# Kernel tuning notes

Hardware: AMD Instinct MI355X
Metric: run time of the kernel (lower is better)

## Reference

```python
import jax, jax.numpy as jnp
import numpy as np

N, K, GS = 11008, 4096, 128   # outfeatures, infeatures, group_size
INTER, KSTRIDE = 4, 64        # interleave, kstride from pack_intweight
B, S = 4, 2048
NG = K // GS                  # number of quantization groups


def _pack_np(q):
    """Replicates torch pack_intweight on an (N, K) int array of 4-bit values."""
    P = q.reshape(N, K // 32, 32)
    P = P.reshape(N, K // 32, 4, 4, 2).transpose(0, 1, 3, 2, 4).reshape(N, K // 32, 32)
    P = P.reshape(N, K // 32, 4, 8).reshape(N, K // 32, 4, 4, 2)
    P = P.transpose(0, 1, 2, 4, 3).reshape(N, K)
    P = P.reshape(N // INTER, INTER, K // KSTRIDE, KSTRIDE).transpose(0, 2, 1, 3)
    P = P.reshape(N // INTER, K // KSTRIDE, KSTRIDE, INTER)
    P = P[..., 0] | (P[..., 1] << 4) | (P[..., 2] << 8) | (P[..., 3] << 12)
    # uint16 bit pattern stored in int32 (schema has no int16)
    return P.reshape(N // INTER, K).astype(np.int32)


def setup_inputs() -> dict:
    rng = np.random.default_rng(0)
    q_unpacked = rng.integers(0, 16, size=(N, K), dtype=np.int64)  # int4 codes
    qweight = jnp.asarray(_pack_np(q_unpacked))

    key = jax.random.key(0)
    k1, k2, k3, k4 = jax.random.split(key, 4)
    x = jax.random.normal(k1, (B, S, K), dtype=jnp.float16)
    scales = (jax.random.uniform(k2, (NG, N), dtype=jnp.float32) * 0.01 + 0.005).astype(jnp.float16)
    scaled_zeros = (jax.random.normal(k3, (NG, N), dtype=jnp.float32) * 0.05).astype(jnp.float16)
    bias = (jax.random.normal(k4, (N,), dtype=jnp.float32) * 0.02).astype(jnp.float16)
    return {"x": x, "qweight": qweight, "scales": scales,
            "scaled_zeros": scaled_zeros, "bias": bias}


def _unpack(qweight):
    """Inverse of pack_intweight: (N//4, K) packed -> (N, K) int4 codes."""
    # split the 4 nibbles packed per 16-bit word
    nib = jnp.stack([(qweight >> (4 * i)) & 0xF for i in range(4)], axis=-1)  # (N//4, K, 4)
    # invert the interleave/kstride step
    t = nib.reshape(N // INTER, K // KSTRIDE, INTER, KSTRIDE)
    t = t.transpose(0, 2, 1, 3).reshape(N, K)
    # invert the second 32-lane shuffle
    t = t.reshape(N, K // 32, 4, 2, 4).transpose(0, 1, 2, 4, 3).reshape(N, K // 32, 32)
    # invert the first 32-lane shuffle
    t = t.reshape(N, K // 32, 4, 4, 2).transpose(0, 1, 3, 2, 4).reshape(N, K)
    return t


def reference(x, qweight, scales, scaled_zeros, bias):
    q = _unpack(qweight).astype(jnp.float16)                      # (N, K) codes 0..15
    s = scales.T[:, :, None]                                      # (N, NG, 1)
    z = scaled_zeros.T[:, :, None]                                # (N, NG, 1); stored as -zero*scale
    # w = q * scale + scaled_zeros  (== (q - zero) * scale)
    W = (q.reshape(N, NG, GS) * s + z).reshape(N, K)              # fp16 dequant
    return jnp.einsum('bsk,nk->bsn', x, W) + bias                 # (B, S, N)
```

## Files before the change

### kernel.cpp

```cpp
#include <hip/hip_runtime.h>
#include <hip/hip_bf16.h>

#define K_TOT 4096
#define N_TOT 11008
#define LDP 72

typedef __bf16 bf16x8 __attribute__((ext_vector_type(8)));
typedef float  f32x4  __attribute__((ext_vector_type(4)));
typedef float  f32x8  __attribute__((ext_vector_type(8)));

typedef __attribute__((address_space(1))) unsigned gu32;
typedef __attribute__((address_space(3))) unsigned lu32;

__device__ __forceinline__ void gload_lds16(const void* g, void* l) {
    __builtin_amdgcn_global_load_lds((gu32*)g, (lu32*)l, 16, 0, 0);
}

__global__ __launch_bounds__(256)
void dequant_w(const int* __restrict__ Qw, const float* __restrict__ Sc,
               const float* __restrict__ Zr, __bf16* __restrict__ Wb)
{
    const int t   = blockIdx.x * 256 + threadIdx.x;
    const int c8  = t & (K_TOT / 8 - 1);
    const int r4  = t >> 9;
    const int kp0 = c8 * 8;
    const int n   = r4 * 4 + ((kp0 >> 4) & 3);
    const int kq  = kp0 >> 6;
    const int hf  = (kp0 >> 3) & 1;
    const int kb  = kq * 64 + hf * 32;

    const int4 wa = *(const int4*)(Qw + (size_t)r4 * K_TOT + kp0);
    const int4 wb = *(const int4*)(Qw + (size_t)r4 * K_TOT + kp0 + 4);
    const int g = kb >> 7;
    const float s = Sc[(size_t)g * N_TOT + n];
    const float z = Zr[(size_t)g * N_TOT + n];

    const int w8[8] = {wa.x, wa.y, wa.z, wa.w, wb.x, wb.y, wb.z, wb.w};
    bf16x8 ov[4];
    #pragma unroll
    for (int uu = 0; uu < 8; ++uu) {
        const unsigned v = (unsigned)w8[uu] & 0xFFFFu;
        #pragma unroll
        for (int i = 0; i < 4; ++i)
            ov[i][uu] = (__bf16)fmaf((float)((v >> (4 * i)) & 0xFu), s, z);
    }
    __bf16* o = Wb + (size_t)n * K_TOT + kb;
    #pragma unroll
    for (int i = 0; i < 4; ++i) *(bf16x8*)(o + i * 8) = ov[i];
}

__global__ __launch_bounds__(256)
void convert_x(const float* __restrict__ X, __bf16* __restrict__ Xb, long total8)
{
    const long t = (long)blockIdx.x * 256 + threadIdx.x;
    if (t >= total8) return;
    f32x8 v = *(const f32x8*)(X + t * 8);
    bf16x8 o;
    #pragma unroll
    for (int j = 0; j < 8; ++j) o[j] = (__bf16)v[j];
    *(bf16x8*)(Xb + t * 8) = o;
}

#define STG_A(kt, kh, bp) do {                                                    \
    const __bf16* g_ = apg + (size_t)(kt) * 64 + (kh) * 32;                       \
    gload_lds16(g_,                       (bp) + (kh) * 16384 + wid * 2048);      \
    gload_lds16(g_ + 16 * (size_t)K_TOT,  (bp) + (kh) * 16384 + wid * 2048 + 1024); \
} while (0)
#define STG_B(kt, kh, bp) do {                                                    \
    const __bf16* g_ = bpg + (size_t)(kt) * 64 + (kh) * 32;                       \
    gload_lds16(g_,                       (bp) + 32768 + (kh) * 16384 + wid * 2048); \
    gload_lds16(g_ + 16 * (size_t)K_TOT,  (bp) + 32768 + (kh) * 16384 + wid * 2048 + 1024); \
} while (0)

#define PH(MH, KK, READB, STGSTMT, GATESTMT)                                      \
  {                                                                               \
    bf16x8 af_[4];                                                                \
    _Pragma("unroll")                                                             \
    for (int j = 0; j < 4; ++j)                                                   \
      af_[j] = *(const bf16x8*)(cur + (KK) * 16384 +                              \
                 (wm + ((MH) * 4 + j) * 16 + l15) * 64 + sw4);                    \
    if (READB) {                                                                  \
      _Pragma("unroll")                                                           \
      for (int n = 0; n < 4; ++n)                                                 \
        bq[n] = *(const bf16x8*)(cur + 32768 + (KK) * 16384 +                     \
                  (wn + n * 16 + l15) * 64 + sw4);                                \
    }                                                                             \
    STGSTMT;                                                                      \
    __builtin_amdgcn_s_barrier();                                                 \
    asm volatile("s_waitcnt lgkmcnt(0)" ::: "memory");                            \
    __builtin_amdgcn_sched_barrier(0);                                            \
    __builtin_amdgcn_s_setprio(1);                                                \
    _Pragma("unroll")                                                             \
    for (int j = 0; j < 4; ++j) {                                                 \
      _Pragma("unroll")                                                           \
      for (int n = 0; n < 4; ++n)                                                 \
        acc[(MH) * 4 + j][n] = __builtin_amdgcn_mfma_f32_16x16x32_bf16(           \
            af_[j], bq[n], acc[(MH) * 4 + j][n], 0, 0, 0);                        \
    }                                                                             \
    __builtin_amdgcn_s_setprio(0);                                                \
    GATESTMT;                                                                     \
    __builtin_amdgcn_s_barrier();                                                 \
  }

#define VM4 asm volatile("s_waitcnt vmcnt(4)" ::: "memory")

__global__ __launch_bounds__(512, 1)
void gemm256p4(const __bf16* __restrict__ A, const __bf16* __restrict__ B,
               const float* __restrict__ Bias, float* __restrict__ C, int gridM)
{
    extern __shared__ char lds_raw[];

    const int tid  = threadIdx.x;
    const int lane = tid & 63;
    const int wid  = tid >> 6;
    const int l15  = lane & 15;
    const int lhi  = lane >> 4;

    const int nwg = gridDim.x;
    int wg = blockIdx.x;
    wg = (wg & 7) * (nwg >> 3) + (wg >> 3);
    const int bx  = wg % gridM;
    const int by  = wg / gridM;
    const int bm0 = bx * 256;
    const int bn0 = by * 256;

    const int wm = (wid >> 2) * 128;
    const int wn = (wid & 3) * 64;

    const int srow  = lane >> 2;
    const int sslot = ((lane & 3) ^ ((srow >> 1) & 3)) * 8;
    const __bf16* apg = A + (size_t)(bm0 + wid * 32 + srow) * K_TOT + sslot;
    const __bf16* bpg = B + (size_t)(bn0 + wid * 32 + srow) * K_TOT + sslot;

    const int sw4 = ((lhi ^ ((l15 >> 1) & 3)) << 4);

    char* cur = lds_raw;
    char* nxt = lds_raw + 65536;

    f32x4 acc[8][4] = {};
    bf16x8 bq[4];

    STG_A(0, 0, cur); STG_B(0, 0, cur);
    STG_A(0, 1, cur); STG_B(0, 1, cur);
    VM4;
    __builtin_amdgcn_s_barrier();

    const int NT = K_TOT / 64;
    for (int t = 0; t < NT; ++t) {
        const int kn = (t + 1 < NT) ? t + 1 : NT - 1;
        PH(0, 0, true,  STG_A(kn, 0, nxt), (void)0)
        PH(1, 0, false, STG_B(kn, 0, nxt), VM4)
        PH(0, 1, true,  STG_A(kn, 1, nxt), (void)0)
        PH(1, 1, false, STG_B(kn, 1, nxt), VM4)
        char* tmp = cur; cur = nxt; nxt = tmp;
    }

    #pragma unroll
    for (int ni = 0; ni < 4; ++ni) {
        const int col = bn0 + wn + ni * 16 + l15;
        const float bv = Bias[col];
        #pragma unroll
        for (int mi = 0; mi < 8; ++mi) {
            const int row = bm0 + wm + mi * 16 + lhi * 4;
            #pragma unroll
            for (int r = 0; r < 4; ++r)
                C[(size_t)(row + r) * N_TOT + col] = acc[mi][ni][r] + bv;
        }
    }
}

__global__ __launch_bounds__(256)
void qgemm_fused(const float* __restrict__ X, const int* __restrict__ Qw,
                 const float* __restrict__ Sc, const float* __restrict__ Zr,
                 const float* __restrict__ Bias, float* __restrict__ C)
{
    __shared__ __bf16 As[128][LDP];
    __shared__ __bf16 Bs[128][LDP];

    const int tid  = threadIdx.x;
    const int lane = tid & 63;
    const int wid  = tid >> 6;
    const int l15  = lane & 15;
    const int lhi  = lane >> 4;

    const int bm0 = blockIdx.x * 128;
    const int bn0 = blockIdx.y * 128;
    const int wm  = (wid >> 1) * 64;
    const int wn  = (wid & 1) * 64;

    const int ar = tid >> 3;
    const int ac = (tid & 7) * 8;

    const int nl   = tid >> 1;
    const int half = tid & 1;
    const int n_g  = bn0 + nl;
    const int* qptr = Qw + (size_t)(n_g >> 2) * K_TOT + (nl & 3) * 16 + half * 8;
    const float* scp = Sc + n_g;
    const float* zrp = Zr + n_g;

    f32x4 acc[4][4] = {};

    for (int kt = 0; kt < K_TOT / 64; ++kt) {
        const int k0 = kt * 64;
        const int4 wa = *(const int4*)(qptr + k0);
        const int4 wb = *(const int4*)(qptr + k0 + 4);
        const float s = scp[(size_t)(kt >> 1) * N_TOT];
        const float z = zrp[(size_t)(kt >> 1) * N_TOT];

        f32x8 av[4];
        #pragma unroll
        for (int p = 0; p < 4; ++p)
            av[p] = *(const f32x8*)(X + (size_t)(bm0 + p * 32 + ar) * K_TOT + k0 + ac);

        const int w8[8] = {wa.x, wa.y, wa.z, wa.w, wb.x, wb.y, wb.z, wb.w};
        bf16x8 ov[4];
        #pragma unroll
        for (int uu = 0; uu < 8; ++uu) {
            const unsigned v = (unsigned)w8[uu] & 0xFFFFu;
            #pragma unroll
            for (int i = 0; i < 4; ++i)
                ov[i][uu] = (__bf16)fmaf((float)((v >> (4 * i)) & 0xFu), s, z);
        }
        #pragma unroll
        for (int p = 0; p < 4; ++p) {
            bf16x8 ab;
            #pragma unroll
            for (int j = 0; j < 8; ++j) ab[j] = (__bf16)av[p][j];
            *(bf16x8*)&As[p * 32 + ar][ac] = ab;
        }
        #pragma unroll
        for (int cc = 0; cc < 4; ++cc)
            *(bf16x8*)&Bs[nl][half * 32 + cc * 8] = ov[cc];

        __syncthreads();

        #pragma unroll
        for (int ks = 0; ks < 2; ++ks) {
            bf16x8 af[4], bfr[4];
            const int kc = ks * 32 + lhi * 8;
            #pragma unroll
            for (int mi = 0; mi < 4; ++mi)
                af[mi] = *(const bf16x8*)&As[wm + mi * 16 + l15][kc];
            #pragma unroll
            for (int ni = 0; ni < 4; ++ni)
                bfr[ni] = *(const bf16x8*)&Bs[wn + ni * 16 + l15][kc];
            #pragma unroll
            for (int mi = 0; mi < 4; ++mi)
                #pragma unroll
                for (int ni = 0; ni < 4; ++ni)
                    acc[mi][ni] = __builtin_amdgcn_mfma_f32_16x16x32_bf16(
                        af[mi], bfr[ni], acc[mi][ni], 0, 0, 0);
        }
        __syncthreads();
    }

    #pragma unroll
    for (int ni = 0; ni < 4; ++ni) {
        const int col = bn0 + wn + ni * 16 + l15;
        const float bv = Bias[col];
        #pragma unroll
        for (int mi = 0; mi < 4; ++mi) {
            const int row = bm0 + wm + mi * 16 + lhi * 4;
            #pragma unroll
            for (int r = 0; r < 4; ++r)
                C[(size_t)(row + r) * N_TOT + col] = acc[mi][ni][r] + bv;
        }
    }
}

extern "C" void kernel_launch(void* const* d_in, const int* in_sizes, int n_in,
                              void* d_out, int out_size, void* d_ws, size_t ws_size,
                              hipStream_t stream) {
    const float* X    = (const float*)d_in[0];
    const int*   Qw   = (const int*)d_in[1];
    const float* Sc   = (const float*)d_in[2];
    const float* Zr   = (const float*)d_in[3];
    const float* Bias = (const float*)d_in[4];
    float* C = (float*)d_out;

    const int M = in_sizes[0] / K_TOT;
    const size_t xb_bytes = (size_t)M * K_TOT * 2;
    const size_t wb_bytes = (size_t)N_TOT * K_TOT * 2;
    const size_t need = xb_bytes + wb_bytes;

    const int gridM = M / 256;
    const int nwg   = gridM * (N_TOT / 256);

    if (ws_size >= need && (M & 255) == 0 && (nwg & 7) == 0) {
        __bf16* Xb = (__bf16*)d_ws;
        __bf16* Wb = (__bf16*)((char*)d_ws + xb_bytes);

        const int nW = (N_TOT / 4) * (K_TOT / 8);
        dequant_w<<<nW / 256, 256, 0, stream>>>(Qw, Sc, Zr, Wb);

        const long total8 = (long)M * K_TOT / 8;
        convert_x<<<(int)((total8 + 255) / 256), 256, 0, stream>>>(X, Xb, total8);

        (void)hipFuncSetAttribute((const void*)gemm256p4,
                                  hipFuncAttributeMaxDynamicSharedMemorySize, 131072);
        gemm256p4<<<dim3(nwg), dim3(512), 131072, stream>>>(Xb, Wb, Bias, C, gridM);
    } else {
        dim3 grid(M / 128, N_TOT / 128);
        qgemm_fused<<<grid, dim3(256), 0, stream>>>(X, Qw, Sc, Zr, Bias, C);
    }
}
```

Before: 936.3 us.

## Restructure bf16 GEMM main loop into register-double-buffered ping-pong schedule

Rewrites the 256x256 bf16 GEMM inner loop to keep two sets of A/B fragments in registers. LDS reads for the next quadrant of MFMAs are issued while the current quadrant computes, and global-to-LDS staging is spread across finer phases with partial lgkmcnt/vmcnt waits. The loop processes two K tiles per iteration and changes the staging order so the first two A tiles are prefetched. This aims to hide LDS read latency behind MFMAs and cut full waits. In exchange it raises register pressure and makes the hand-tuned barrier and wait counts harder to get right.

```diff
diff --git a/kernel.cpp b/kernel.cpp
--- a/kernel.cpp
+++ b/kernel.cpp
@@ -72,40 +72,41 @@
     gload_lds16(g_ + 16 * (size_t)K_TOT,  (bp) + 32768 + (kh) * 16384 + wid * 2048 + 1024); \
 } while (0)
 
-#define PH(MH, KK, READB, STGSTMT, GATESTMT)                                      \
-  {                                                                               \
-    bf16x8 af_[4];                                                                \
+#define RD_A(dst, buf, G0)                                                        \
     _Pragma("unroll")                                                             \
-    for (int j = 0; j < 4; ++j)                                                   \
-      af_[j] = *(const bf16x8*)(cur + (KK) * 16384 +                              \
-                 (wm + ((MH) * 4 + j) * 16 + l15) * 64 + sw4);                    \
-    if (READB) {                                                                  \
+    for (int j_ = 0; j_ < 4; ++j_)                                                \
       _Pragma("unroll")                                                           \
-      for (int n = 0; n < 4; ++n)                                                 \
-        bq[n] = *(const bf16x8*)(cur + 32768 + (KK) * 16384 +                     \
-                  (wn + n * 16 + l15) * 64 + sw4);                                \
-    }                                                                             \
-    STGSTMT;                                                                      \
-    __builtin_amdgcn_s_barrier();                                                 \
-    asm volatile("s_waitcnt lgkmcnt(0)" ::: "memory");                            \
-    __builtin_amdgcn_sched_barrier(0);                                            \
+      for (int kk_ = 0; kk_ < 2; ++kk_)                                           \
+        dst[j_][kk_] = *(const bf16x8*)((buf) + kk_ * 16384 +                     \
+                        (wm + ((G0) + j_) * 16 + l15) * 64 + sw4);
+
+#define RD_B(dst, buf, N0)                                                        \
+    _Pragma("unroll")                                                             \
+    for (int n_ = 0; n_ < 2; ++n_)                                                \
+      _Pragma("unroll")                                                           \
+      for (int kk_ = 0; kk_ < 2; ++kk_)                                           \
+        dst[n_][kk_] = *(const bf16x8*)((buf) + 32768 + kk_ * 16384 +             \
+                        (wn + ((N0) + n_) * 16 + l15) * 64 + sw4);
+
+#define MM(R0, C0, Aset, Bset)                                                    \
     __builtin_amdgcn_s_setprio(1);                                                \
     _Pragma("unroll")                                                             \
-    for (int j = 0; j < 4; ++j) {                                                 \
+    for (int mi_ = 0; mi_ < 4; ++mi_)                                             \
       _Pragma("unroll")                                                           \
-      for (int n = 0; n < 4; ++n)                                                 \
-        acc[(MH) * 4 + j][n] = __builtin_amdgcn_mfma_f32_16x16x32_bf16(           \
-            af_[j], bq[n], acc[(MH) * 4 + j][n], 0, 0, 0);                        \
-    }                                                                             \
-    __builtin_amdgcn_s_setprio(0);                                                \
-    GATESTMT;                                                                     \
-    __builtin_amdgcn_s_barrier();                                                 \
-  }
-
-#define VM4 asm volatile("s_waitcnt vmcnt(4)" ::: "memory")
+      for (int n_ = 0; n_ < 2; ++n_)                                              \
+        _Pragma("unroll")                                                         \
+        for (int kk_ = 0; kk_ < 2; ++kk_)                                         \
+          acc[(R0) + mi_][(C0) + n_] = __builtin_amdgcn_mfma_f32_16x16x32_bf16(   \
+              Aset[mi_][kk_], Bset[n_][kk_], acc[(R0) + mi_][(C0) + n_], 0, 0, 0);\
+    __builtin_amdgcn_s_setprio(0);
+
+#define BAR      __builtin_amdgcn_s_barrier()
+#define SBAR     __builtin_amdgcn_sched_barrier(0)
+#define LGKM(n)  asm volatile("s_waitcnt lgkmcnt(" #n ")" ::: "memory")
+#define VM2      asm volatile("s_waitcnt vmcnt(2)" ::: "memory")
 
 __global__ __launch_bounds__(512, 1)
-void gemm256p4(const __bf16* __restrict__ A, const __bf16* __restrict__ B,
+void gemm256ra(const __bf16* __restrict__ A, const __bf16* __restrict__ B,
                const float* __restrict__ Bias, float* __restrict__ C, int gridM)
 {
     extern __shared__ char lds_raw[];
@@ -134,25 +135,63 @@
 
     const int sw4 = ((lhi ^ ((l15 >> 1) & 3)) << 4);
 
-    char* cur = lds_raw;
-    char* nxt = lds_raw + 65536;
+    char* buf0 = lds_raw;
+    char* buf1 = lds_raw + 65536;
 
     f32x4 acc[8][4] = {};
-    bf16x8 bq[4];
-
-    STG_A(0, 0, cur); STG_B(0, 0, cur);
-    STG_A(0, 1, cur); STG_B(0, 1, cur);
-    VM4;
-    __builtin_amdgcn_s_barrier();
-
-    const int NT = K_TOT / 64;
-    for (int t = 0; t < NT; ++t) {
-        const int kn = (t + 1 < NT) ? t + 1 : NT - 1;
-        PH(0, 0, true,  STG_A(kn, 0, nxt), (void)0)
-        PH(1, 0, false, STG_B(kn, 0, nxt), VM4)
-        PH(0, 1, true,  STG_A(kn, 1, nxt), (void)0)
-        PH(1, 1, false, STG_B(kn, 1, nxt), VM4)
-        char* tmp = cur; cur = nxt; nxt = tmp;
+    bf16x8 a0[4][2], a1[4][2], b0[2][2], b1[2][2];
+
+    STG_A(0, 0, buf0); STG_A(0, 1, buf0);
+    STG_B(0, 0, buf0); STG_B(0, 1, buf0);
+    STG_A(1, 0, buf1); STG_A(1, 1, buf1);
+    asm volatile("s_waitcnt vmcnt(4)" ::: "memory");
+    BAR;
+    RD_A(a0, buf0, 0);
+    RD_B(b0, buf0, 0);
+
+    const int NT  = K_TOT / 64;
+    const int NIT = NT / 2;
+    for (int i = 0; i < NIT; ++i) {
+        const int tQ = 2 * i + 1;
+        const int tR = (2 * i + 2 < NT) ? 2 * i + 2 : NT - 1;
+        const int tS = (2 * i + 3 < NT) ? 2 * i + 3 : NT - 1;
+
+        RD_A(a1, buf0, 4);
+        STG_B(tQ, 0, buf1);
+        BAR; LGKM(8); SBAR;
+        MM(0, 0, a0, b0);
+        RD_B(b1, buf0, 2);
+        STG_B(tQ, 1, buf1);
+        BAR; LGKM(4); SBAR;
+        MM(4, 0, a1, b0);
+        STG_A(tR, 0, buf0);
+        BAR; LGKM(0); SBAR;
+        MM(4, 2, a1, b1);
+        VM2;
+        STG_A(tR, 1, buf0);
+        BAR;
+        RD_A(a1, buf1, 0);
+        RD_B(b0, buf1, 0);
+        LGKM(12); SBAR;
+        MM(0, 2, a0, b1);
+        RD_A(a0, buf1, 4);
+        STG_B(tR, 0, buf0);
+        BAR; LGKM(8); SBAR;
+        MM(0, 0, a1, b0);
+        RD_B(b1, buf1, 2);
+        STG_B(tR, 1, buf0);
+        BAR; LGKM(4); SBAR;
+        MM(4, 0, a0, b0);
+        STG_A(tS, 0, buf1);
+        BAR; LGKM(0); SBAR;
+        MM(4, 2, a0, b1);
+        VM2;
+        STG_A(tS, 1, buf1);
+        BAR;
+        RD_A(a0, buf0, 0);
+        RD_B(b0, buf0, 0);
+        LGKM(12); SBAR;
+        MM(0, 2, a1, b1);
     }
 
     #pragma unroll
@@ -296,9 +335,9 @@
         const long total8 = (long)M * K_TOT / 8;
         convert_x<<<(int)((total8 + 255) / 256), 256, 0, stream>>>(X, Xb, total8);
 
-        (void)hipFuncSetAttribute((const void*)gemm256p4,
+        (void)hipFuncSetAttribute((const void*)gemm256ra,
                                   hipFuncAttributeMaxDynamicSharedMemorySize, 131072);
-        gemm256p4<<<dim3(nwg), dim3(512), 131072, stream>>>(Xb, Wb, Bias, C, gridM);
+        gemm256ra<<<dim3(nwg), dim3(512), 131072, stream>>>(Xb, Wb, Bias, C, gridM);
     } else {
         dim3 grid(M / 128, N_TOT / 128);
         qgemm_fused<<<grid, dim3(256), 0, stream>>>(X, Qw, Sc, Zr, Bias, C);
```

After: 927.6 us. About the same (-0.9%).
